# Kernel optimization log

Measured on AMD Instinct MI355X. Metric: run time of the kernel, lower is better.

Reference implementation:

```python
import jax, jax.numpy as jnp
import numpy as np

E_EDGES = 100000   # number of original edges (edge tokens)
M_PAIRS = 1000000  # number of edge-edge (line-graph) pairs
IN_DIM = 128
H = 8   # num_heads
D = 16  # out_dim per head


def setup_inputs() -> dict:
    key = jax.random.key(0)
    ks = jax.random.split(key, 8)
    edge_attr = jax.random.normal(ks[0], (E_EDGES, IN_DIM), dtype=jnp.float32)
    edge_edge_index = jax.random.randint(ks[1], (2, M_PAIRS), 0, E_EDGES, dtype=jnp.int64)
    s = 1.0 / np.sqrt(IN_DIM)  # xavier-ish scale
    Wq = jax.random.normal(ks[2], (IN_DIM, H * D), dtype=jnp.float32) * s
    Wk = jax.random.normal(ks[3], (IN_DIM, H * D), dtype=jnp.float32) * s
    Wv = jax.random.normal(ks[4], (IN_DIM, H * D), dtype=jnp.float32) * s
    bq = jnp.zeros((H * D,), dtype=jnp.float32)
    bk = jnp.zeros((H * D,), dtype=jnp.float32)
    bv = jnp.zeros((H * D,), dtype=jnp.float32)
    Aw = jax.random.normal(ks[5], (D, H), dtype=jnp.float32) * (1.0 / np.sqrt(D))
    return {"edge_attr": edge_attr, "edge_edge_index": edge_edge_index,
            "Wq": Wq, "bq": bq, "Wk": Wk, "bk": bk, "Wv": Wv, "bv": bv, "Aw": Aw}


def reference(edge_attr, edge_edge_index, Wq, bq, Wk, bk, Wv, bv, Aw):
    E = edge_attr.shape[0]
    # Q/K/V projections, reshaped to [E, H, D]
    Qh = (edge_attr @ Wq + bq).reshape(E, H, D)
    Kh = (edge_attr @ Wk + bk).reshape(E, H, D)
    Vh = (edge_attr @ Wv + bv).reshape(E, H, D)
    src = edge_edge_index[0]
    dst = edge_edge_index[1]
    # gather + additive score over edge-edge pairs: [M, H, D]
    score_vec = Kh[src] + Qh[dst]  # act = Identity
    # einsum 'ehd,dhc->ehc' with c=1 -> [M, H]
    raw_attn = jnp.einsum('mhd,dh->mh', score_vec, Aw)
    # segment softmax grouped by destination edge
    mx = jax.ops.segment_max(raw_attn, dst, num_segments=E)  # [E, H]
    ex = jnp.exp(raw_attn - mx[dst])
    denom = jax.ops.segment_sum(ex, dst, num_segments=E)[dst] + 1e-16
    attn = ex / denom  # [M, H]; dropout p=0 -> identity
    # weighted scatter-add aggregation
    msg = Vh[src] * attn[..., None]  # [M, H, D]
    edge_out = jax.ops.segment_sum(msg, dst, num_segments=E)  # [E, H, D]
    return edge_out
```

## Files before the change

### kernel.cpp

```cpp
#include <hip/hip_runtime.h>
#include <math.h>

static constexpr int E = 100000;
static constexpr int M = 1000000;
static constexpr int NBE = (E + 255) / 256;
static constexpr int NBM = (M + 255) / 256;
static constexpr int NBP = (E + 63) / 64;
static constexpr int NBM4 = (M + 1023) / 1024;
static constexpr int NZC = (E / 4 + 255) / 256;

#define O_FLAG   0
#define O_WEFF   512
#define O_BKEFF  4608
#define O_BSWZ   5120
#define O_COUNTS 38400
#define O_OFFS   438784
#define O_BSUM   838784
#define O_BSUM2  840832
#define O_BINOFF 842880
#define O_GBIN   843904
#define O_ORDER  852096
#define O_POS    1252096
#define O_CSR    5252096
#define O_WS     9252096
#define O_VH     12452096
#define WS_NEEDED (O_VH + (size_t)E * 128 * 2)

typedef float f32x4 __attribute__((ext_vector_type(4)));
typedef short s16x8 __attribute__((ext_vector_type(8)));

__device__ __forceinline__ unsigned short f2bf(float f) {
    unsigned u = __float_as_uint(f);
    u += 0x7fffu + ((u >> 16) & 1u);
    return (unsigned short)(u >> 16);
}
__device__ __forceinline__ float bflo(unsigned u) { return __uint_as_float(u << 16); }
__device__ __forceinline__ float bfhi(unsigned u) { return __uint_as_float(u & 0xffff0000u); }

__device__ __forceinline__ int weswz(int k) { return (k ^ ((k >> 3) & 3)) << 3; }

__global__ void k_prep(const float* __restrict__ Wk, const float* __restrict__ bk,
                       const float* __restrict__ Aw, const float* __restrict__ Wv,
                       const int* __restrict__ idx32, int* __restrict__ flag,
                       float* __restrict__ weff, float* __restrict__ bkeff,
                       unsigned short* __restrict__ Bswz, uint4* __restrict__ countsz,
                       uint4* __restrict__ gbinz) {
    int bid = blockIdx.x, t = threadIdx.x;
    if (bid < NZC) {
        int i4 = bid * 256 + t;
        if (i4 < E / 4) countsz[i4] = make_uint4(0, 0, 0, 0);
        return;
    }
    if (bid == NZC) {
        __shared__ float sAw[128];
        if (t < 128) sAw[t] = Aw[t];
        __syncthreads();
#pragma unroll
        for (int j = 0; j < 4; j++) {
            int o = t + 256 * j;
            int row = o >> 3, h = o & 7;
            float s = 0.f;
#pragma unroll
            for (int d = 0; d < 16; d++) s += Wk[row * 128 + h * 16 + d] * sAw[d * 8 + h];
            weff[o] = s;
        }
        if (t < 8) {
            float s = 0.f;
            for (int d = 0; d < 16; d++) s += bk[t * 16 + d] * sAw[d * 8 + t];
            bkeff[t] = s;
        }
        return;
    }
    if (bid == NZC + 1) {
        uint4 z = make_uint4(0, 0, 0, 0);
        gbinz[t] = z; gbinz[t + 256] = z;
        if (t == 0) {
            int zc = 0;
            for (int i = 0; i < 64; i++) zc += (idx32[2 * i + 1] == 0) ? 1 : 0;
            *flag = (zc == 64) ? 1 : 0;
        }
        return;
    }
    int p = (bid - (NZC + 2)) * 256 + t;
    int f = p >> 6, lane = p & 63;
    int c = f >> 3, tt = f & 7;
    int quad = lane >> 4, nn = lane & 15;
#pragma unroll
    for (int j = 0; j < 8; j++) {
        int k = c * 32 + quad * 8 + j;
        Bswz[p * 8 + j] = f2bf(Wv[k * 128 + tt * 16 + nn]);
    }
}

__global__ __launch_bounds__(256) void k_count(
    const void* __restrict__ idx, const int* __restrict__ flagp,
    int* __restrict__ counts, int* __restrict__ pos) {
    int t = threadIdx.x;
    int base = blockIdx.x * 1024 + t;
    int m0 = base, m1 = base + 256, m2 = base + 512, m3 = base + 768;
    int d0 = 0, d1 = 0, d2 = 0, d3 = 0;
    if (*flagp) {
        const long long* p = (const long long*)idx;
        if (m0 < M) d0 = (int)p[M + m0];
        if (m1 < M) d1 = (int)p[M + m1];
        if (m2 < M) d2 = (int)p[M + m2];
        if (m3 < M) d3 = (int)p[M + m3];
    } else {
        const int* p = (const int*)idx;
        if (m0 < M) d0 = p[M + m0];
        if (m1 < M) d1 = p[M + m1];
        if (m2 < M) d2 = p[M + m2];
        if (m3 < M) d3 = p[M + m3];
    }
    if (m0 < M) pos[m0] = atomicAdd(&counts[d0], 1);
    if (m1 < M) pos[m1] = atomicAdd(&counts[d1], 1);
    if (m2 < M) pos[m2] = atomicAdd(&counts[d2], 1);
    if (m3 < M) pos[m3] = atomicAdd(&counts[d3], 1);
}

__global__ __launch_bounds__(256) void k_proj(
    const float* __restrict__ A, const short* __restrict__ Bswz,
    const float* __restrict__ bv, const float* __restrict__ weff,
    const float* __restrict__ bkeff, unsigned short* __restrict__ Vh,
    float* __restrict__ wsb) {
    int t = threadIdx.x;
    int pid = blockIdx.x;

    __shared__ float we[1024];
    {
        int k = t >> 1;
        int off = weswz(k) + ((t & 1) << 2);
        *(float4*)&we[off] = ((const float4*)weff)[t];
    }
    __syncthreads();

    int lane = t & 63, wid = t >> 6;
    int rowbase = pid * 64 + wid * 16;
    int quad = lane >> 4, nn = lane & 15;
    int m = rowbase + nn;
    int mc = (m < E) ? m : (E - 1);

    f32x4 acc[8];
#pragma unroll
    for (int tt = 0; tt < 8; tt++) acc[tt] = (f32x4){0.f, 0.f, 0.f, 0.f};
    float p[8];
#pragma unroll
    for (int h = 0; h < 8; h++) p[h] = 0.f;

#pragma unroll
    for (int c = 0; c < 4; c++) {
        const float4* ap = (const float4*)(A + (size_t)mc * 128 + c * 32 + quad * 8);
        float4 f0 = ap[0], f1 = ap[1];
        float a[8] = {f0.x, f0.y, f0.z, f0.w, f1.x, f1.y, f1.z, f1.w};
#pragma unroll
        for (int j = 0; j < 8; j++) {
            int k = c * 32 + quad * 8 + j;
            int kb = weswz(k);
            float4 w0 = *(const float4*)&we[kb];
            float4 w1 = *(const float4*)&we[kb + 4];
            p[0] += a[j] * w0.x; p[1] += a[j] * w0.y;
            p[2] += a[j] * w0.z; p[3] += a[j] * w0.w;
            p[4] += a[j] * w1.x; p[5] += a[j] * w1.y;
            p[6] += a[j] * w1.z; p[7] += a[j] * w1.w;
        }
        s16x8 afrag;
#pragma unroll
        for (int j = 0; j < 8; j++) afrag[j] = (short)f2bf(a[j]);
#pragma unroll
        for (int tt = 0; tt < 8; tt++) {
            s16x8 bfrag = *(const s16x8*)(Bswz + (((c * 8 + tt) * 64 + lane) << 3));
            acc[tt] = __builtin_amdgcn_mfma_f32_16x16x32_bf16(afrag, bfrag, acc[tt], 0, 0, 0);
        }
    }
#pragma unroll
    for (int off = 16; off <= 32; off <<= 1)
#pragma unroll
        for (int h = 0; h < 8; h++) p[h] += __shfl_xor(p[h], off, 64);
    if (quad == 0 && m < E) {
        float4* op = (float4*)(wsb + (size_t)m * 8);
        op[0] = make_float4(__expf(p[0] + bkeff[0]), __expf(p[1] + bkeff[1]),
                            __expf(p[2] + bkeff[2]), __expf(p[3] + bkeff[3]));
        op[1] = make_float4(__expf(p[4] + bkeff[4]), __expf(p[5] + bkeff[5]),
                            __expf(p[6] + bkeff[6]), __expf(p[7] + bkeff[7]));
    }
#pragma unroll
    for (int tt = 0; tt < 8; tt++) {
        float bvc = bv[tt * 16 + nn];
#pragma unroll
        for (int rr = 0; rr < 4; rr++) {
            int row = rowbase + quad * 4 + rr;
            if (row < E)
                Vh[(size_t)row * 128 + tt * 16 + nn] = f2bf(acc[tt][rr] + bvc);
        }
    }
}

__global__ void k_scanA(int* __restrict__ counts, int* __restrict__ offs,
                        int* __restrict__ bsum, int* __restrict__ gbin) {
    __shared__ int sm[256];
    __shared__ int lh[256];
    __shared__ int bb[256];
    int tid = threadIdx.x;
    int i = blockIdx.x * 256 + tid;
    int v = (i < E) ? counts[i] : 0;
    int n = v > 255 ? 255 : v;
    lh[tid] = 0;
    sm[tid] = v;
    __syncthreads();
    int lr = 0;
    if (i < E) lr = atomicAdd(&lh[n], 1);
    for (int off = 1; off < 256; off <<= 1) {
        int add = (tid >= off) ? sm[tid - off] : 0;
        __syncthreads();
        sm[tid] += add;
        __syncthreads();
    }
    if (i < E) offs[i] = sm[tid] - v;
    if (tid == 255) bsum[blockIdx.x] = sm[255];
    int cnt = lh[tid];
    if (cnt > 0) bb[tid] = atomicAdd(&gbin[tid * 8], cnt);
    __syncthreads();
    if (i < E) counts[i] = ((bb[n] + lr) << 8) | n;
}

__global__ void k_scanB2(const int* __restrict__ bsum, const int* __restrict__ gbin,
                         int* __restrict__ bsum2, int* __restrict__ binoff, int nb) {
    __shared__ int sm[512];
    __shared__ int s2[256];
    int tid = threadIdx.x;
    int v = (tid < nb) ? bsum[tid] : 0;
    sm[tid] = v;
    __syncthreads();
    for (int off = 1; off < 512; off <<= 1) {
        int add = (tid >= off) ? sm[tid - off] : 0;
        __syncthreads();
        sm[tid] += add;
        __syncthreads();
    }
    bsum2[tid] = sm[tid] - v;
    int bv = 0;
    if (tid < 256) { bv = gbin[(255 - tid) * 8]; s2[tid] = bv; }
    __syncthreads();
    for (int off = 1; off < 256; off <<= 1) {
        int add = (tid < 256 && tid >= off) ? s2[tid - off] : 0;
        __syncthreads();
        if (tid < 256) s2[tid] += add;
        __syncthreads();
    }
    if (tid < 256) binoff[255 - tid] = s2[tid] - bv;
}

__global__ void k_fill(const void* __restrict__ idx, const int* __restrict__ flagp,
                       const int* __restrict__ offs, const int* __restrict__ bsum2,
                       const int* __restrict__ pos, int* __restrict__ csr,
                       const int* __restrict__ counts, const int* __restrict__ binoff,
                       int* __restrict__ order) {
    int bid = blockIdx.x, t = threadIdx.x;
    if (bid < NBM) {
        int m = bid * 256 + t;
        if (m >= M) return;
        int s, d;
        if (*flagp) {
            const long long* p = (const long long*)idx;
            s = (int)p[m]; d = (int)p[M + m];
        } else {
            const int* p = (const int*)idx;
            s = p[m]; d = p[M + m];
        }
        csr[offs[d] + bsum2[d >> 8] + pos[m]] = s;
        return;
    }
    int i = (bid - NBM) * 256 + t;
    if (i >= E) return;
    int v = counts[i];
    order[binoff[v & 255] + (v >> 8)] = i;
}

#define ROWL(p, sidx, cond) \
    if (cond) { \
        k##p = wsb[(size_t)(sidx) * 8 + h]; \
        const uint4* vp_ = (const uint4*)(Vh + (size_t)(sidx) * 128 + (h << 4)); \
        a##p = vp_[0]; b##p = vp_[1]; \
    }

#define CONS(kk, aa, bb) { \
    float w_ = kk; \
    l += w_; \
    acc[0]  += bflo(aa.x) * w_; acc[1]  += bfhi(aa.x) * w_; \
    acc[2]  += bflo(aa.y) * w_; acc[3]  += bfhi(aa.y) * w_; \
    acc[4]  += bflo(aa.z) * w_; acc[5]  += bfhi(aa.z) * w_; \
    acc[6]  += bflo(aa.w) * w_; acc[7]  += bfhi(aa.w) * w_; \
    acc[8]  += bflo(bb.x) * w_; acc[9]  += bfhi(bb.x) * w_; \
    acc[10] += bflo(bb.y) * w_; acc[11] += bfhi(bb.y) * w_; \
    acc[12] += bflo(bb.z) * w_; acc[13] += bfhi(bb.z) * w_; \
    acc[14] += bflo(bb.w) * w_; acc[15] += bfhi(bb.w) * w_; \
}

__global__ __launch_bounds__(256) void k_seg(
    const float* __restrict__ wsb, const unsigned short* __restrict__ Vh,
    const int* __restrict__ offs, const int* __restrict__ bsum2,
    const int* __restrict__ csr, const int* __restrict__ order,
    float* __restrict__ out) {
    int t = threadIdx.x;
    int h = t & 7;
    int g = blockIdx.x * 32 + (t >> 3);
    int seg = order[g];
    int beg = offs[seg] + bsum2[seg >> 8];
    int end = (seg + 1 < E) ? (offs[seg + 1] + bsum2[(seg + 1) >> 8]) : M;
    int n = end - beg;

    float acc[16];
#pragma unroll
    for (int j = 0; j < 16; j++) acc[j] = 0.f;
    float l = 0.f;

    if (n > 0) {
        int s0 = 0, s1 = 0, s2 = 0, s3 = 0, t0 = 0, t1 = 0, t2 = 0, t3 = 0;
        float k0 = 0, k1 = 0, k2 = 0, k3 = 0;
        uint4 a0 = {}, b0 = {}, a1 = {}, b1 = {}, a2 = {}, b2 = {}, a3 = {}, b3 = {};
        s0 = csr[beg];
        if (n > 1) s1 = csr[beg + 1];
        if (n > 2) s2 = csr[beg + 2];
        if (n > 3) s3 = csr[beg + 3];
        ROWL(0, s0, true)
        ROWL(1, s1, n > 1)
        ROWL(2, s2, n > 2)
        ROWL(3, s3, n > 3)
        if (n > 4) t0 = csr[beg + 4];
        if (n > 5) t1 = csr[beg + 5];
        if (n > 6) t2 = csr[beg + 6];
        if (n > 7) t3 = csr[beg + 7];
        int i = 0;
        while (i + 4 <= n) {
            CONS(k0, a0, b0) ROWL(0, t0, i + 4 < n) if (i + 8 < n)  t0 = csr[beg + i + 8];
            CONS(k1, a1, b1) ROWL(1, t1, i + 5 < n) if (i + 9 < n)  t1 = csr[beg + i + 9];
            CONS(k2, a2, b2) ROWL(2, t2, i + 6 < n) if (i + 10 < n) t2 = csr[beg + i + 10];
            CONS(k3, a3, b3) ROWL(3, t3, i + 7 < n) if (i + 11 < n) t3 = csr[beg + i + 11];
            i += 4;
        }
        if (i < n) { CONS(k0, a0, b0) i++; }
        if (i < n) { CONS(k1, a1, b1) i++; }
        if (i < n) { CONS(k2, a2, b2) }
    }
    float inv = 1.0f / (l + 1e-16f);
    float4* op = (float4*)(out + (size_t)seg * 128 + h * 16);
#pragma unroll
    for (int j = 0; j < 4; j++)
        op[j] = make_float4(acc[4 * j] * inv, acc[4 * j + 1] * inv,
                            acc[4 * j + 2] * inv, acc[4 * j + 3] * inv);
}

extern "C" void kernel_launch(void* const* d_in, const int* in_sizes, int n_in,
                              void* d_out, int out_size, void* d_ws, size_t ws_size,
                              hipStream_t stream) {
    const float* edge_attr = (const float*)d_in[0];
    const void*  eei       = d_in[1];
    const float* Wk = (const float*)d_in[4];
    const float* bk = (const float*)d_in[5];
    const float* Wv = (const float*)d_in[6];
    const float* bv = (const float*)d_in[7];
    const float* Aw = (const float*)d_in[8];
    float* out = (float*)d_out;

    if (ws_size < WS_NEEDED) return;

    char* ws = (char*)d_ws;
    int*   flag   = (int*)(ws + O_FLAG);
    float* weff   = (float*)(ws + O_WEFF);
    float* bkeff  = (float*)(ws + O_BKEFF);
    unsigned short* Bswz = (unsigned short*)(ws + O_BSWZ);
    int*   counts = (int*)(ws + O_COUNTS);
    int*   offs   = (int*)(ws + O_OFFS);
    int*   bsum   = (int*)(ws + O_BSUM);
    int*   bsum2  = (int*)(ws + O_BSUM2);
    int*   binoff = (int*)(ws + O_BINOFF);
    int*   gbin   = (int*)(ws + O_GBIN);
    int*   order  = (int*)(ws + O_ORDER);
    int*   pos    = (int*)(ws + O_POS);
    int*   csr    = (int*)(ws + O_CSR);
    float* wsb    = (float*)(ws + O_WS);
    unsigned short* Vh = (unsigned short*)(ws + O_VH);

    k_prep<<<NZC + 10, 256, 0, stream>>>(Wk, bk, Aw, Wv, (const int*)eei, flag,
                                         weff, bkeff, Bswz, (uint4*)counts,
                                         (uint4*)gbin);
    k_count<<<NBM4, 256, 0, stream>>>(eei, flag, counts, pos);
    k_proj<<<NBP, 256, 0, stream>>>(edge_attr, (const short*)Bswz, bv, weff,
                                    bkeff, Vh, wsb);
    k_scanA<<<NBE, 256, 0, stream>>>(counts, offs, bsum, gbin);
    k_scanB2<<<1, 512, 0, stream>>>(bsum, gbin, bsum2, binoff, NBE);
    k_fill<<<NBM + NBE, 256, 0, stream>>>(eei, flag, offs, bsum2, pos, csr,
                                          counts, binoff, order);
    k_seg<<<E / 32, 256, 0, stream>>>(wsb, Vh, offs, bsum2, csr, order, out);
}
```

Before: 273.0 us.

## Fuse count and projection kernels; switch Vh and weights to head-major layout

Merges the atomic counting kernel and the projection kernel into one launch that interleaves their blocks 2:3, so the memory-bound atomics can overlap with the MFMA projection. Stores Vh and the exp-weights head-major ([H][E][16] and [H][E]). The segment kernel now gives each block a single head and one segment per thread, so the gathered rows for a given head come from a smaller per-head region that may cache better. The trade-offs are less coalesced scattered writes in the projection and heavier per-thread work in the segment kernel, with one lane per segment instead of eight.

```diff
diff --git a/kernel.cpp b/kernel.cpp
--- a/kernel.cpp
+++ b/kernel.cpp
@@ -92,39 +92,42 @@
     }
 }
 
-__global__ __launch_bounds__(256) void k_count(
+__global__ __launch_bounds__(256) void k_cp(
     const void* __restrict__ idx, const int* __restrict__ flagp,
-    int* __restrict__ counts, int* __restrict__ pos) {
-    int t = threadIdx.x;
-    int base = blockIdx.x * 1024 + t;
-    int m0 = base, m1 = base + 256, m2 = base + 512, m3 = base + 768;
-    int d0 = 0, d1 = 0, d2 = 0, d3 = 0;
-    if (*flagp) {
-        const long long* p = (const long long*)idx;
-        if (m0 < M) d0 = (int)p[M + m0];
-        if (m1 < M) d1 = (int)p[M + m1];
-        if (m2 < M) d2 = (int)p[M + m2];
-        if (m3 < M) d3 = (int)p[M + m3];
-    } else {
-        const int* p = (const int*)idx;
-        if (m0 < M) d0 = p[M + m0];
-        if (m1 < M) d1 = p[M + m1];
-        if (m2 < M) d2 = p[M + m2];
-        if (m3 < M) d3 = p[M + m3];
-    }
-    if (m0 < M) pos[m0] = atomicAdd(&counts[d0], 1);
-    if (m1 < M) pos[m1] = atomicAdd(&counts[d1], 1);
-    if (m2 < M) pos[m2] = atomicAdd(&counts[d2], 1);
-    if (m3 < M) pos[m3] = atomicAdd(&counts[d3], 1);
-}
-
-__global__ __launch_bounds__(256) void k_proj(
+    int* __restrict__ counts, int* __restrict__ pos,
     const float* __restrict__ A, const short* __restrict__ Bswz,
     const float* __restrict__ bv, const float* __restrict__ weff,
     const float* __restrict__ bkeff, unsigned short* __restrict__ Vh,
     float* __restrict__ wsb) {
-    int t = threadIdx.x;
-    int pid = blockIdx.x;
+    int bid = blockIdx.x, t = threadIdx.x;
+    int r = bid % 5;
+    if (r < 2) {
+        int cid = (bid / 5) * 2 + r;
+        if (cid >= NBM4) return;
+        int base = cid * 1024 + t;
+        int m0 = base, m1 = base + 256, m2 = base + 512, m3 = base + 768;
+        int d0 = 0, d1 = 0, d2 = 0, d3 = 0;
+        if (*flagp) {
+            const long long* p = (const long long*)idx;
+            if (m0 < M) d0 = (int)p[M + m0];
+            if (m1 < M) d1 = (int)p[M + m1];
+            if (m2 < M) d2 = (int)p[M + m2];
+            if (m3 < M) d3 = (int)p[M + m3];
+        } else {
+            const int* p = (const int*)idx;
+            if (m0 < M) d0 = p[M + m0];
+            if (m1 < M) d1 = p[M + m1];
+            if (m2 < M) d2 = p[M + m2];
+            if (m3 < M) d3 = p[M + m3];
+        }
+        if (m0 < M) pos[m0] = atomicAdd(&counts[d0], 1);
+        if (m1 < M) pos[m1] = atomicAdd(&counts[d1], 1);
+        if (m2 < M) pos[m2] = atomicAdd(&counts[d2], 1);
+        if (m3 < M) pos[m3] = atomicAdd(&counts[d3], 1);
+        return;
+    }
+    int pid = (bid / 5) * 3 + (r - 2);
+    if (pid >= NBP) return;
 
     __shared__ float we[1024];
     {
@@ -177,11 +180,9 @@
 #pragma unroll
         for (int h = 0; h < 8; h++) p[h] += __shfl_xor(p[h], off, 64);
     if (quad == 0 && m < E) {
-        float4* op = (float4*)(wsb + (size_t)m * 8);
-        op[0] = make_float4(__expf(p[0] + bkeff[0]), __expf(p[1] + bkeff[1]),
-                            __expf(p[2] + bkeff[2]), __expf(p[3] + bkeff[3]));
-        op[1] = make_float4(__expf(p[4] + bkeff[4]), __expf(p[5] + bkeff[5]),
-                            __expf(p[6] + bkeff[6]), __expf(p[7] + bkeff[7]));
+#pragma unroll
+        for (int h = 0; h < 8; h++)
+            wsb[(size_t)h * E + m] = __expf(p[h] + bkeff[h]);
     }
 #pragma unroll
     for (int tt = 0; tt < 8; tt++) {
@@ -190,7 +191,7 @@
         for (int rr = 0; rr < 4; rr++) {
             int row = rowbase + quad * 4 + rr;
             if (row < E)
-                Vh[(size_t)row * 128 + tt * 16 + nn] = f2bf(acc[tt][rr] + bvc);
+                Vh[((size_t)tt * E + row) * 16 + nn] = f2bf(acc[tt][rr] + bvc);
         }
     }
 }
@@ -278,8 +279,8 @@
 
 #define ROWL(p, sidx, cond) \
     if (cond) { \
-        k##p = wsb[(size_t)(sidx) * 8 + h]; \
-        const uint4* vp_ = (const uint4*)(Vh + (size_t)(sidx) * 128 + (h << 4)); \
+        k##p = wh[sidx]; \
+        const uint4* vp_ = (const uint4*)(vh + ((size_t)(sidx) << 4)); \
         a##p = vp_[0]; b##p = vp_[1]; \
     }
 
@@ -301,13 +302,17 @@
     const int* __restrict__ offs, const int* __restrict__ bsum2,
     const int* __restrict__ csr, const int* __restrict__ order,
     float* __restrict__ out) {
-    int t = threadIdx.x;
-    int h = t & 7;
-    int g = blockIdx.x * 32 + (t >> 3);
+    int bid = blockIdx.x;
+    int h = bid & 7;
+    int g = (bid >> 3) * 256 + threadIdx.x;
+    if (g >= E) return;
     int seg = order[g];
     int beg = offs[seg] + bsum2[seg >> 8];
     int end = (seg + 1 < E) ? (offs[seg + 1] + bsum2[(seg + 1) >> 8]) : M;
     int n = end - beg;
+
+    const float* wh = wsb + (size_t)h * E;
+    const unsigned short* vh = Vh + (size_t)h * E * 16;
 
     float acc[16];
 #pragma unroll
@@ -384,12 +389,11 @@
     k_prep<<<NZC + 10, 256, 0, stream>>>(Wk, bk, Aw, Wv, (const int*)eei, flag,
                                          weff, bkeff, Bswz, (uint4*)counts,
                                          (uint4*)gbin);
-    k_count<<<NBM4, 256, 0, stream>>>(eei, flag, counts, pos);
-    k_proj<<<NBP, 256, 0, stream>>>(edge_attr, (const short*)Bswz, bv, weff,
-                                    bkeff, Vh, wsb);
+    k_cp<<<5 * 521, 256, 0, stream>>>(eei, flag, counts, pos, edge_attr,
+                                      (const short*)Bswz, bv, weff, bkeff, Vh, wsb);
     k_scanA<<<NBE, 256, 0, stream>>>(counts, offs, bsum, gbin);
     k_scanB2<<<1, 512, 0, stream>>>(bsum, gbin, bsum2, binoff, NBE);
     k_fill<<<NBM + NBE, 256, 0, stream>>>(eei, flag, offs, bsum2, pos, csr,
                                           counts, binoff, order);
-    k_seg<<<E / 32, 256, 0, stream>>>(wsb, Vh, offs, bsum2, csr, order, out);
-}
+    k_seg<<<NBE * 8, 256, 0, stream>>>(wsb, Vh, offs, bsum2, csr, order, out);
+}
```

After: 340.3 us. 1.25x slower.

## Fuse count with projection, use cursor atomics in fill, split segments across two lanes

Applied to the files above, without the earlier changes.

The edge-counting pass and the V/K projection now run in one launch: every fourth block counts destinations with atomics and the rest do projection, so the two overlap. The per-pair position array is dropped. The fill pass instead claims CSR slots with atomic increments on a per-segment cursor written by the scan, which trades a pos write and read for extra atomics and makes the order within a segment nondeterministic. The segment kernel gives each segment to two 8-lane halves that take alternate pairs and combine results with shuffles, exposing more parallelism for long segments.

```diff
diff --git a/kernel.cpp b/kernel.cpp
--- a/kernel.cpp
+++ b/kernel.cpp
@@ -6,7 +6,8 @@
 static constexpr int NBE = (E + 255) / 256;
 static constexpr int NBM = (M + 255) / 256;
 static constexpr int NBP = (E + 63) / 64;
-static constexpr int NBM4 = (M + 1023) / 1024;
+static constexpr int NBM8 = (M + 2047) / 2048;
+static constexpr int GCNT = 521;
 static constexpr int NZC = (E / 4 + 255) / 256;
 
 #define O_FLAG   0
@@ -20,7 +21,7 @@
 #define O_BINOFF 842880
 #define O_GBIN   843904
 #define O_ORDER  852096
-#define O_POS    1252096
+#define O_CUR    1252096
 #define O_CSR    5252096
 #define O_WS     9252096
 #define O_VH     12452096
@@ -92,39 +93,38 @@
     }
 }
 
-__global__ __launch_bounds__(256) void k_count(
+__global__ __launch_bounds__(256) void k_cp(
     const void* __restrict__ idx, const int* __restrict__ flagp,
-    int* __restrict__ counts, int* __restrict__ pos) {
-    int t = threadIdx.x;
-    int base = blockIdx.x * 1024 + t;
-    int m0 = base, m1 = base + 256, m2 = base + 512, m3 = base + 768;
-    int d0 = 0, d1 = 0, d2 = 0, d3 = 0;
-    if (*flagp) {
-        const long long* p = (const long long*)idx;
-        if (m0 < M) d0 = (int)p[M + m0];
-        if (m1 < M) d1 = (int)p[M + m1];
-        if (m2 < M) d2 = (int)p[M + m2];
-        if (m3 < M) d3 = (int)p[M + m3];
-    } else {
-        const int* p = (const int*)idx;
-        if (m0 < M) d0 = p[M + m0];
-        if (m1 < M) d1 = p[M + m1];
-        if (m2 < M) d2 = p[M + m2];
-        if (m3 < M) d3 = p[M + m3];
-    }
-    if (m0 < M) pos[m0] = atomicAdd(&counts[d0], 1);
-    if (m1 < M) pos[m1] = atomicAdd(&counts[d1], 1);
-    if (m2 < M) pos[m2] = atomicAdd(&counts[d2], 1);
-    if (m3 < M) pos[m3] = atomicAdd(&counts[d3], 1);
-}
-
-__global__ __launch_bounds__(256) void k_proj(
+    int* __restrict__ counts,
     const float* __restrict__ A, const short* __restrict__ Bswz,
     const float* __restrict__ bv, const float* __restrict__ weff,
     const float* __restrict__ bkeff, unsigned short* __restrict__ Vh,
     float* __restrict__ wsb) {
-    int t = threadIdx.x;
-    int pid = blockIdx.x;
+    int bid = blockIdx.x, t = threadIdx.x;
+    int r = bid & 3;
+    if (r == 0) {
+        int cid = bid >> 2;
+        if (cid >= NBM8) return;
+        int base = cid * 2048 + t;
+        if (*flagp) {
+            const long long* p = (const long long*)idx;
+#pragma unroll
+            for (int k = 0; k < 8; k++) {
+                int m = base + k * 256;
+                if (m < M) atomicAdd(&counts[(int)p[M + m]], 1);
+            }
+        } else {
+            const int* p = (const int*)idx;
+#pragma unroll
+            for (int k = 0; k < 8; k++) {
+                int m = base + k * 256;
+                if (m < M) atomicAdd(&counts[p[M + m]], 1);
+            }
+        }
+        return;
+    }
+    int pid = (bid >> 2) * 3 + (r - 1);
+    if (pid >= NBP) return;
 
     __shared__ float we[1024];
     {
@@ -196,7 +196,8 @@
 }
 
 __global__ void k_scanA(int* __restrict__ counts, int* __restrict__ offs,
-                        int* __restrict__ bsum, int* __restrict__ gbin) {
+                        int* __restrict__ cur, int* __restrict__ bsum,
+                        int* __restrict__ gbin) {
     __shared__ int sm[256];
     __shared__ int lh[256];
     __shared__ int bb[256];
@@ -215,7 +216,7 @@
         sm[tid] += add;
         __syncthreads();
     }
-    if (i < E) offs[i] = sm[tid] - v;
+    if (i < E) { offs[i] = sm[tid] - v; cur[i] = sm[tid] - v; }
     if (tid == 255) bsum[blockIdx.x] = sm[255];
     int cnt = lh[tid];
     if (cnt > 0) bb[tid] = atomicAdd(&gbin[tid * 8], cnt);
@@ -251,8 +252,8 @@
 }
 
 __global__ void k_fill(const void* __restrict__ idx, const int* __restrict__ flagp,
-                       const int* __restrict__ offs, const int* __restrict__ bsum2,
-                       const int* __restrict__ pos, int* __restrict__ csr,
+                       int* __restrict__ cur, const int* __restrict__ bsum2,
+                       int* __restrict__ csr,
                        const int* __restrict__ counts, const int* __restrict__ binoff,
                        int* __restrict__ order) {
     int bid = blockIdx.x, t = threadIdx.x;
@@ -267,7 +268,8 @@
             const int* p = (const int*)idx;
             s = p[m]; d = p[M + m];
         }
-        csr[offs[d] + bsum2[d >> 8] + pos[m]] = s;
+        int slot = atomicAdd(&cur[d], 1) + bsum2[d >> 8];
+        csr[slot] = s;
         return;
     }
     int i = (bid - NBM) * 256 + t;
@@ -302,52 +304,60 @@
     const int* __restrict__ csr, const int* __restrict__ order,
     float* __restrict__ out) {
     int t = threadIdx.x;
-    int h = t & 7;
-    int g = blockIdx.x * 32 + (t >> 3);
+    int lane16 = t & 15;
+    int h = lane16 & 7;
+    int part = lane16 >> 3;
+    int g = blockIdx.x * 16 + (t >> 4);
     int seg = order[g];
     int beg = offs[seg] + bsum2[seg >> 8];
     int end = (seg + 1 < E) ? (offs[seg + 1] + bsum2[(seg + 1) >> 8]) : M;
     int n = end - beg;
+    int np = (n - part + 1) >> 1;
+    int base = beg + part;
 
     float acc[16];
 #pragma unroll
     for (int j = 0; j < 16; j++) acc[j] = 0.f;
     float l = 0.f;
 
-    if (n > 0) {
+    if (np > 0) {
         int s0 = 0, s1 = 0, s2 = 0, s3 = 0, t0 = 0, t1 = 0, t2 = 0, t3 = 0;
         float k0 = 0, k1 = 0, k2 = 0, k3 = 0;
         uint4 a0 = {}, b0 = {}, a1 = {}, b1 = {}, a2 = {}, b2 = {}, a3 = {}, b3 = {};
-        s0 = csr[beg];
-        if (n > 1) s1 = csr[beg + 1];
-        if (n > 2) s2 = csr[beg + 2];
-        if (n > 3) s3 = csr[beg + 3];
+        s0 = csr[base];
+        if (np > 1) s1 = csr[base + 2];
+        if (np > 2) s2 = csr[base + 4];
+        if (np > 3) s3 = csr[base + 6];
         ROWL(0, s0, true)
-        ROWL(1, s1, n > 1)
-        ROWL(2, s2, n > 2)
-        ROWL(3, s3, n > 3)
-        if (n > 4) t0 = csr[beg + 4];
-        if (n > 5) t1 = csr[beg + 5];
-        if (n > 6) t2 = csr[beg + 6];
-        if (n > 7) t3 = csr[beg + 7];
+        ROWL(1, s1, np > 1)
+        ROWL(2, s2, np > 2)
+        ROWL(3, s3, np > 3)
+        if (np > 4) t0 = csr[base + 8];
+        if (np > 5) t1 = csr[base + 10];
+        if (np > 6) t2 = csr[base + 12];
+        if (np > 7) t3 = csr[base + 14];
         int i = 0;
-        while (i + 4 <= n) {
-            CONS(k0, a0, b0) ROWL(0, t0, i + 4 < n) if (i + 8 < n)  t0 = csr[beg + i + 8];
-            CONS(k1, a1, b1) ROWL(1, t1, i + 5 < n) if (i + 9 < n)  t1 = csr[beg + i + 9];
-            CONS(k2, a2, b2) ROWL(2, t2, i + 6 < n) if (i + 10 < n) t2 = csr[beg + i + 10];
-            CONS(k3, a3, b3) ROWL(3, t3, i + 7 < n) if (i + 11 < n) t3 = csr[beg + i + 11];
+        while (i + 4 <= np) {
+            CONS(k0, a0, b0) ROWL(0, t0, i + 4 < np) if (i + 8 < np)  t0 = csr[base + 2 * (i + 8)];
+            CONS(k1, a1, b1) ROWL(1, t1, i + 5 < np) if (i + 9 < np)  t1 = csr[base + 2 * (i + 9)];
+            CONS(k2, a2, b2) ROWL(2, t2, i + 6 < np) if (i + 10 < np) t2 = csr[base + 2 * (i + 10)];
+            CONS(k3, a3, b3) ROWL(3, t3, i + 7 < np) if (i + 11 < np) t3 = csr[base + 2 * (i + 11)];
             i += 4;
         }
-        if (i < n) { CONS(k0, a0, b0) i++; }
-        if (i < n) { CONS(k1, a1, b1) i++; }
-        if (i < n) { CONS(k2, a2, b2) }
-    }
+        if (i < np) { CONS(k0, a0, b0) i++; }
+        if (i < np) { CONS(k1, a1, b1) i++; }
+        if (i < np) { CONS(k2, a2, b2) }
+    }
+    l += __shfl_xor(l, 8, 64);
+#pragma unroll
+    for (int j = 0; j < 16; j++) acc[j] += __shfl_xor(acc[j], 8, 64);
     float inv = 1.0f / (l + 1e-16f);
-    float4* op = (float4*)(out + (size_t)seg * 128 + h * 16);
-#pragma unroll
-    for (int j = 0; j < 4; j++)
-        op[j] = make_float4(acc[4 * j] * inv, acc[4 * j + 1] * inv,
-                            acc[4 * j + 2] * inv, acc[4 * j + 3] * inv);
+    float4* op = (float4*)(out + (size_t)seg * 128 + h * 16 + part * 8);
+    int ab = part * 8;
+    op[0] = make_float4(acc[ab] * inv, acc[ab + 1] * inv,
+                        acc[ab + 2] * inv, acc[ab + 3] * inv);
+    op[1] = make_float4(acc[ab + 4] * inv, acc[ab + 5] * inv,
+                        acc[ab + 6] * inv, acc[ab + 7] * inv);
 }
 
 extern "C" void kernel_launch(void* const* d_in, const int* in_sizes, int n_in,
@@ -376,7 +386,7 @@
     int*   binoff = (int*)(ws + O_BINOFF);
     int*   gbin   = (int*)(ws + O_GBIN);
     int*   order  = (int*)(ws + O_ORDER);
-    int*   pos    = (int*)(ws + O_POS);
+    int*   cur    = (int*)(ws + O_CUR);
     int*   csr    = (int*)(ws + O_CSR);
     float* wsb    = (float*)(ws + O_WS);
     unsigned short* Vh = (unsigned short*)(ws + O_VH);
@@ -384,12 +394,11 @@
     k_prep<<<NZC + 10, 256, 0, stream>>>(Wk, bk, Aw, Wv, (const int*)eei, flag,
                                          weff, bkeff, Bswz, (uint4*)counts,
                                          (uint4*)gbin);
-    k_count<<<NBM4, 256, 0, stream>>>(eei, flag, counts, pos);
-    k_proj<<<NBP, 256, 0, stream>>>(edge_attr, (const short*)Bswz, bv, weff,
-                                    bkeff, Vh, wsb);
-    k_scanA<<<NBE, 256, 0, stream>>>(counts, offs, bsum, gbin);
+    k_cp<<<4 * GCNT, 256, 0, stream>>>(eei, flag, counts, edge_attr,
+                                       (const short*)Bswz, bv, weff, bkeff, Vh, wsb);
+    k_scanA<<<NBE, 256, 0, stream>>>(counts, offs, cur, bsum, gbin);
     k_scanB2<<<1, 512, 0, stream>>>(bsum, gbin, bsum2, binoff, NBE);
-    k_fill<<<NBM + NBE, 256, 0, stream>>>(eei, flag, offs, bsum2, pos, csr,
+    k_fill<<<NBM + NBE, 256, 0, stream>>>(eei, flag, cur, bsum2, csr,
                                           counts, binoff, order);
-    k_seg<<<E / 32, 256, 0, stream>>>(wsb, Vh, offs, bsum2, csr, order, out);
-}
+    k_seg<<<E / 16, 256, 0, stream>>>(wsb, Vh, offs, bsum2, csr, order, out);
+}
```

Result: slower. 292.3 us (+7.1%).
